# Performance work log

Hardware: AMD Instinct MI355X
Metric: run time of the kernel (lower is better)

The kernel has to match this reference:

```python
import jax, jax.numpy as jnp
import numpy as np

H = 64          # hiddenNum
C3 = 3 * H      # 192 attention channels
FL = 7          # filterLen
PAD = FL // 2
NORM = 1.0 / np.sqrt(C3).astype(np.float32)


def _u(key, shape, stdv):
    return jax.random.uniform(key, shape, jnp.float32, -stdv, stdv)


def setup_inputs() -> dict:
    key = jax.random.key(0)
    ks = iter(jax.random.split(key, 64))
    B, N = 16, 1024
    x = jax.random.normal(next(ks), (B, N, 128), jnp.float32)
    adj = jax.random.uniform(next(ks), (B, N, N), jnp.float32)
    degree = jax.random.uniform(next(ks), (B, N, N), jnp.float32)
    eps = jax.random.normal(next(ks), (B, C3), jnp.float32) * 0.1
    d = {"x": x, "adj": adj, "degree": degree, "eps": eps}
    # GCN params (torch uniform(-1/sqrt(out), 1/sqrt(out)))
    for name, fi, fo in [("gcn1", 128, 2 * H), ("gcn2", H, 4 * H), ("gcn3", 2 * H, 6 * H)]:
        s = 1.0 / np.sqrt(fo)
        d[name + "_w"] = _u(next(ks), (fi, fo), s)
        d[name + "_b"] = _u(next(ks), (fo,), s)
    # Conv1d params [out, in, k]
    for name, ci, co in [("conv1", 128, 2 * H), ("conv2", H, 4 * H), ("conv3", 2 * H, 6 * H)]:
        s = 1.0 / np.sqrt(ci * FL)
        d[name + "_w"] = _u(next(ks), (co, ci, FL), s)
        d[name + "_b"] = _u(next(ks), (co,), s)
    # 1x1 conv Q/K/V projections
    s = 1.0 / np.sqrt(C3)
    for name in ["srq", "srk", "srv", "drq", "drk", "drv"]:
        d[name + "_w"] = _u(next(ks), (C3, C3, 1), s)
        d[name + "_b"] = _u(next(ks), (C3,), s)
    # Linear layers [out, in]
    for name in ["l1", "l2"]:
        d[name + "_w"] = _u(next(ks), (C3, C3), s)
        d[name + "_b"] = _u(next(ks), (C3,), s)
    return d


def _glu_last(y):
    o, g = jnp.split(y, 2, axis=-1)
    return o * jax.nn.sigmoid(g)


def _glu_ch(y):
    o, g = jnp.split(y, 2, axis=1)
    return o * jax.nn.sigmoid(g)


def _conv1d(x, w, b, pad):
    y = jax.lax.conv_general_dilated(x, w, (1,), [(pad, pad)],
                                     dimension_numbers=("NCH", "OIH", "NCH"))
    return y + b[None, :, None]


def reference(x, adj, degree, eps,
              gcn1_w, gcn1_b, gcn2_w, gcn2_b, gcn3_w, gcn3_b,
              conv1_w, conv1_b, conv2_w, conv2_b, conv3_w, conv3_b,
              srq_w, srq_b, srk_w, srk_b, srv_w, srv_b,
              drq_w, drq_b, drk_w, drk_b, drv_w, drv_b,
              l1_w, l1_b, l2_w, l2_b):
    # normalized adjacency: D @ A @ D  (batched dense bmm, as in the original)
    adj_n = jnp.matmul(jnp.matmul(degree, adj), degree)  # [B,N,N]

    def gcn(inp, W, b):
        return jnp.matmul(adj_n, inp @ W) + b

    # GCN branch with GLU gating (eval mode: dropout = identity)
    g1 = _glu_last(gcn(x, gcn1_w, gcn1_b))      # [B,N,H]
    g2 = _glu_last(gcn(g1, gcn2_w, gcn2_b))     # [B,N,2H]
    g3 = _glu_last(gcn(g2, gcn3_w, gcn3_b))     # [B,N,3H]
    gcn_out = jnp.transpose(g3, (0, 2, 1))      # [B,3H,N]

    # CNN branch with gated convs
    xc = jnp.transpose(x, (0, 2, 1))            # [B,128,N]
    c1 = _glu_ch(_conv1d(xc, conv1_w, conv1_b, PAD))   # [B,H,N]
    c2 = _glu_ch(_conv1d(c1, conv2_w, conv2_b, PAD))   # [B,2H,N]
    cnn_out = _glu_ch(_conv1d(c2, conv3_w, conv3_b, PAD))  # [B,3H,N]

    # 1x1-conv Q/K/V projections
    def p1x1(t, w, b):
        return jnp.einsum('oc,bcn->bon', w[:, :, 0], t) + b[None, :, None]

    SRQ = p1x1(cnn_out, srq_w, srq_b)
    SRK = p1x1(cnn_out, srk_w, srk_b)
    SRV = p1x1(cnn_out, srv_w, srv_b)
    DRQ = p1x1(gcn_out, drq_w, drq_b)
    DRK = p1x1(gcn_out, drk_w, drk_b)
    DRV = p1x1(gcn_out, drv_w, drv_b)

    # dual cross-attention; NOTE: scale applied AFTER softmax, as in the source
    attSR = jax.nn.softmax(jnp.einsum('bcn,bcm->bnm', SRQ, DRK), axis=-1) * NORM
    outSR = jnp.einsum('bnm,bcm->bnc', attSR, SRV)   # [B,N,3H]
    attDR = jax.nn.softmax(jnp.einsum('bcn,bcm->bnm', DRQ, SRK), axis=-1) * NORM
    outDR = jnp.einsum('bnm,bcm->bnc', attDR, DRV)   # [B,N,3H]

    feat = outSR + outDR                              # [B,N,3H]
    pooled = jnp.mean(feat, axis=1)                   # AdaptiveAvgPool1d(1) over N -> [B,3H]

    out1 = jax.nn.relu(pooled @ l1_w.T + l1_b)        # mean
    out2 = jax.nn.relu(pooled @ l2_w.T + l2_b)        # logvar
    std = jnp.exp(0.5 * out2)
    out0 = eps * std + out1                           # reparametrize
    return (out0, out1, out2)
```

## Files before the change

### kernel.cpp

```cpp
#include <hip/hip_runtime.h>


#define Bn 16
#define Nn 1024
#define C3n 192
static __device__ __constant__ float NORM_C = 0.07216878364870322f;

typedef short bf16x8 __attribute__((ext_vector_type(8)));
typedef float f32x4 __attribute__((ext_vector_type(4)));
typedef unsigned short u16;
typedef unsigned short u16x4 __attribute__((ext_vector_type(4)));

__device__ __forceinline__ u16 bf16rn(float x)
{
  unsigned b = __float_as_uint(x);
  b += 0x7fffu + ((b >> 16) & 1u);
  return (u16)(b >> 16);
}
__device__ __forceinline__ float fromh(u16 h) { return __uint_as_float(((unsigned)h) << 16); }

template<int TM, int TN, bool OUTB, int BIAS, bool ACC, bool OUTT>
__global__ __launch_bounds__(256, 2) void mgemm_k(
    const u16* __restrict__ A, long sA, int lda,
    const u16* __restrict__ B, long sB, int ldb,
    const float* __restrict__ bias,
    float* __restrict__ Cf, u16* __restrict__ Cb,
    int M, int N, int K)
{
  constexpr int WMN = (TM >= 128) ? 2 : 1;
  constexpr int WNN = 4 / WMN;
  constexpr int WTM = TM / WMN, WTN = TN / WNN;
  constexpr int FM = WTM / 16, FN = WTN / 16;
  constexpr int BBASE = TM * 128;
  __shared__ __align__(16) char sm[(TM + TN) * 128];

  const int bz = (int)blockIdx.z;
  const int n0 = blockIdx.x * TN, m0 = blockIdx.y * TM;
  const int tid = threadIdx.x, lane = tid & 63, w = tid >> 6;
  const int wm0 = (w / WNN) * WTM, wn0 = (w % WNN) * WTN;

  bf16x8 rA[TM / 32], rB[TN / 32];
  auto loadA = [&](int k0) {
    const u16* p = A + bz * sA + (long)m0 * lda + k0;
#pragma unroll
    for (int i = 0; i < TM / 32; ++i) {
      const int v = tid + i * 256, row = v >> 3, vc = v & 7;
      rA[i] = *(const bf16x8*)(p + (long)row * lda + vc * 8);
    }
  };
  auto storeA = [&]() {
#pragma unroll
    for (int i = 0; i < TM / 32; ++i) {
      const int v = tid + i * 256, row = v >> 3, vc = v & 7;
      *(bf16x8*)(sm + row * 128 + ((vc * 16) ^ ((row & 7) << 4))) = rA[i];
    }
  };
  auto loadB = [&](int k0) {
    const u16* p = B + bz * sB + (long)n0 * ldb + k0;
#pragma unroll
    for (int i = 0; i < TN / 32; ++i) {
      const int v = tid + i * 256, row = v >> 3, vc = v & 7;
      rB[i] = *(const bf16x8*)(p + (long)row * ldb + vc * 8);
    }
  };
  auto storeB = [&]() {
#pragma unroll
    for (int i = 0; i < TN / 32; ++i) {
      const int v = tid + i * 256, row = v >> 3, vc = v & 7;
      *(bf16x8*)(sm + BBASE + row * 128 + ((vc * 16) ^ ((row & 7) << 4))) = rB[i];
    }
  };

  f32x4 acc[FM][FN];
#pragma unroll
  for (int c = 0; c < FM; ++c)
#pragma unroll
    for (int d = 0; d < FN; ++d) acc[c][d] = (f32x4)(0.0f);

  loadA(0); loadB(0);
  for (int k0 = 0; k0 < K; k0 += 64) {
    storeA(); storeB();
    __syncthreads();
    if (k0 + 64 < K) { loadA(k0 + 64); loadB(k0 + 64); }
#pragma unroll
    for (int s = 0; s < 2; ++s) {
      const int kb = s * 64 + ((lane >> 4) << 4);
      bf16x8 ah[FM], bh[FN];
#pragma unroll
      for (int c = 0; c < FM; ++c) {
        const int ar = wm0 + c * 16 + (lane & 15);
        ah[c] = *(const bf16x8*)(sm + ar * 128 + (kb ^ ((ar & 7) << 4)));
      }
#pragma unroll
      for (int d = 0; d < FN; ++d) {
        const int br = wn0 + d * 16 + (lane & 15);
        bh[d] = *(const bf16x8*)(sm + BBASE + br * 128 + (kb ^ ((br & 7) << 4)));
      }
#pragma unroll
      for (int c = 0; c < FM; ++c)
#pragma unroll
        for (int d = 0; d < FN; ++d)
          acc[c][d] = __builtin_amdgcn_mfma_f32_16x16x32_bf16(ah[c], bh[d], acc[c][d], 0, 0, 0);
    }
    __syncthreads();
  }

  const long cb = (long)bz * M * N;
#pragma unroll
  for (int c = 0; c < FM; ++c)
#pragma unroll
    for (int d = 0; d < FN; ++d) {
      const int row0 = m0 + wm0 + c * 16 + (lane >> 4) * 4;
      const int col = n0 + wn0 + d * 16 + (lane & 15);
      if constexpr (OUTT) {
        u16x4 vv;
#pragma unroll
        for (int r = 0; r < 4; ++r) vv[r] = bf16rn(acc[c][d][r]);
        *(u16x4*)(Cb + cb + (long)col * M + row0) = vv;
      } else {
        float bcol = 0.f;
        if constexpr (BIAS == 1) bcol = bias[col];
#pragma unroll
        for (int r = 0; r < 4; ++r) {
          const int row = row0 + r;
          float v = acc[c][d][r];
          if constexpr (BIAS == 1) v += bcol;
          if constexpr (BIAS == 2) v += bias[row];
          const long idx = cb + (long)row * N + col;
          if constexpr (OUTB) {
            Cb[idx] = bf16rn(v);
          } else {
            if constexpr (ACC) v += Cf[idx];
            Cf[idx] = v;
          }
        }
      }
    }
}

__device__ __forceinline__ void gemm64_body(char* sm,
    const u16* __restrict__ A, int lda, const u16* __restrict__ B, int ldb,
    const float* __restrict__ bias, u16* __restrict__ Cb,
    int N, int K, int m0, int n0, bool biasRow)
{
  const int tid = threadIdx.x, lane = tid & 63, w = tid >> 6;
  bf16x8 rA[2], rB[2];
  auto loadA = [&](int k0) {
#pragma unroll
    for (int i = 0; i < 2; ++i) {
      const int v = tid + i * 256, row = v >> 3, vc = v & 7;
      rA[i] = *(const bf16x8*)(A + (long)(m0 + row) * lda + k0 + vc * 8);
    }
  };
  auto loadB = [&](int k0) {
#pragma unroll
    for (int i = 0; i < 2; ++i) {
      const int v = tid + i * 256, row = v >> 3, vc = v & 7;
      rB[i] = *(const bf16x8*)(B + (long)(n0 + row) * ldb + k0 + vc * 8);
    }
  };
  auto storeAB = [&]() {
#pragma unroll
    for (int i = 0; i < 2; ++i) {
      const int v = tid + i * 256, row = v >> 3, vc = v & 7;
      const int off = row * 128 + ((vc * 16) ^ ((row & 7) << 4));
      *(bf16x8*)(sm + off) = rA[i];
      *(bf16x8*)(sm + 8192 + off) = rB[i];
    }
  };

  f32x4 acc[4];
#pragma unroll
  for (int c = 0; c < 4; ++c) acc[c] = (f32x4)(0.0f);

  loadA(0); loadB(0);
  for (int k0 = 0; k0 < K; k0 += 64) {
    storeAB();
    __syncthreads();
    if (k0 + 64 < K) { loadA(k0 + 64); loadB(k0 + 64); }
#pragma unroll
    for (int s = 0; s < 2; ++s) {
      const int kb = s * 64 + ((lane >> 4) << 4);
      const int br = w * 16 + (lane & 15);
      const bf16x8 bh = *(const bf16x8*)(sm + 8192 + br * 128 + (kb ^ ((br & 7) << 4)));
#pragma unroll
      for (int c = 0; c < 4; ++c) {
        const int ar = c * 16 + (lane & 15);
        const bf16x8 ah = *(const bf16x8*)(sm + ar * 128 + (kb ^ ((ar & 7) << 4)));
        acc[c] = __builtin_amdgcn_mfma_f32_16x16x32_bf16(ah, bh, acc[c], 0, 0, 0);
      }
    }
    __syncthreads();
  }

  const int col = n0 + w * 16 + (lane & 15);
  const float bcol = biasRow ? 0.f : bias[col];
#pragma unroll
  for (int c = 0; c < 4; ++c) {
    const int row0 = m0 + c * 16 + (lane >> 4) * 4;
#pragma unroll
    for (int r = 0; r < 4; ++r) {
      const int row = row0 + r;
      const float bv = biasRow ? bias[row] : bcol;
      Cb[(long)row * N + col] = bf16rn(acc[c][r] + bv);
    }
  }
}

__global__ __launch_bounds__(256, 2) void qk4_k(
    const u16* __restrict__ inA, const u16* __restrict__ inB,
    const u16* __restrict__ w0, const u16* __restrict__ w1,
    const u16* __restrict__ w2, const u16* __restrict__ w3,
    const float* __restrict__ b0, const float* __restrict__ b1,
    const float* __restrict__ b2, const float* __restrict__ b3,
    u16* __restrict__ o0, u16* __restrict__ o1,
    u16* __restrict__ o2, u16* __restrict__ o3)
{
  __shared__ __align__(16) char sm[16384];
  constexpr long QS = (long)Nn * C3n;
  const int z = blockIdx.z, p = z >> 4, b = z & 15;
  const u16* in = (p < 2) ? inA : inB;
  const u16* W = (p == 0) ? w0 : (p == 1) ? w1 : (p == 2) ? w2 : w3;
  const float* bias = (p == 0) ? b0 : (p == 1) ? b1 : (p == 2) ? b2 : b3;
  u16* out = (p == 0) ? o0 : (p == 1) ? o1 : (p == 2) ? o2 : o3;
  gemm64_body(sm, in + (long)b * QS, C3n, W, C3n, bias, out + (long)b * QS,
              C3n, C3n, blockIdx.y * 64, blockIdx.x * 64, false);
}

__global__ __launch_bounds__(256, 2) void v2_k(
    const u16* __restrict__ inA, const u16* __restrict__ inB,
    const u16* __restrict__ w0, const u16* __restrict__ w1,
    const float* __restrict__ b0, const float* __restrict__ b1,
    u16* __restrict__ o0, u16* __restrict__ o1)
{
  __shared__ __align__(16) char sm[16384];
  constexpr long QS = (long)Nn * C3n;
  const int z = blockIdx.z, p = z >> 4, b = z & 15;
  const u16* in = p ? inB : inA;
  const u16* W = p ? w1 : w0;
  const float* bias = p ? b1 : b0;
  u16* out = p ? o1 : o0;
  gemm64_body(sm, W, C3n, in + (long)b * QS, C3n, bias, out + (long)b * QS,
              Nn, C3n, blockIdx.y * 64, blockIdx.x * 64, true);
}

template<int KC, bool OUTT>
__global__ __launch_bounds__(256, 2) void wglu_k(
    const u16* __restrict__ A, long sA,
    const u16* __restrict__ W,
    const float* __restrict__ bias,
    u16* __restrict__ G, long sG, int H)
{
  __shared__ __align__(16) char sm[3 * 8192];
  const int bz = blockIdx.z;
  const int h0 = blockIdx.x * 64, m0 = blockIdx.y * 64;
  const int tid = threadIdx.x, lane = tid & 63, w = tid >> 6;
  const int wn0 = w * 16;

  f32x4 accO[4], accG[4];
#pragma unroll
  for (int c = 0; c < 4; ++c) { accO[c] = (f32x4)(0.0f); accG[c] = (f32x4)(0.0f); }

  for (int k0 = 0; k0 < KC; k0 += 64) {
#pragma unroll
    for (int i = 0; i < 2; ++i) {
      const int v = tid + i * 256, row = v >> 3, vc = v & 7;
      const int off = row * 128 + ((vc * 16) ^ ((row & 7) << 4));
      *(bf16x8*)(sm + off) = *(const bf16x8*)(A + bz * sA + (long)(m0 + row) * KC + k0 + vc * 8);
      *(bf16x8*)(sm + 8192 + off) = *(const bf16x8*)(W + (long)(h0 + row) * KC + k0 + vc * 8);
      *(bf16x8*)(sm + 16384 + off) = *(const bf16x8*)(W + (long)(H + h0 + row) * KC + k0 + vc * 8);
    }
    __syncthreads();
#pragma unroll
    for (int s = 0; s < 2; ++s) {
      const int kb = s * 64 + ((lane >> 4) << 4);
      const int br = wn0 + (lane & 15);
      const bf16x8 bo = *(const bf16x8*)(sm + 8192 + br * 128 + (kb ^ ((br & 7) << 4)));
      const bf16x8 bg = *(const bf16x8*)(sm + 16384 + br * 128 + (kb ^ ((br & 7) << 4)));
#pragma unroll
      for (int c = 0; c < 4; ++c) {
        const int ar = c * 16 + (lane & 15);
        const bf16x8 a = *(const bf16x8*)(sm + ar * 128 + (kb ^ ((ar & 7) << 4)));
        accO[c] = __builtin_amdgcn_mfma_f32_16x16x32_bf16(a, bo, accO[c], 0, 0, 0);
        accG[c] = __builtin_amdgcn_mfma_f32_16x16x32_bf16(a, bg, accG[c], 0, 0, 0);
      }
    }
    __syncthreads();
  }

  const int col = h0 + wn0 + (lane & 15);
  const float bo = bias[col], bg = bias[H + col];
#pragma unroll
  for (int c = 0; c < 4; ++c) {
    const int row0 = m0 + c * 16 + (lane >> 4) * 4;
    if constexpr (OUTT) {
      u16x4 vv;
#pragma unroll
      for (int r = 0; r < 4; ++r) {
        const float o = accO[c][r] + bo, g = accG[c][r] + bg;
        vv[r] = bf16rn(o / (1.f + expf(-g)));
      }
      *(u16x4*)(G + bz * sG + (long)col * Nn + row0) = vv;
    } else {
#pragma unroll
      for (int r = 0; r < 4; ++r) {
        const float o = accO[c][r] + bo, g = accG[c][r] + bg;
        G[bz * sG + (long)(row0 + r) * H + col] = bf16rn(o / (1.f + expf(-g)));
      }
    }
  }
}

__global__ __launch_bounds__(256, 2) void conv_mfma_k(
    const u16* __restrict__ Wp, const u16* __restrict__ in_nm, int ldin, long sIn,
    u16* __restrict__ Z, long sZ, int Ci, int M)
{
  __shared__ __align__(16) char sm[9216 + 7 * 8192];
  const int bz = blockIdx.z;
  const int n0 = blockIdx.x * 64, m0 = blockIdx.y * 64;
  const int tid = threadIdx.x, lane = tid & 63, w = tid >> 6;
  const int wm = (w >> 1) * 32, wn = (w & 1) * 32;
  const u16* inb = in_nm + bz * sIn;

  f32x4 acc[2][2];
#pragma unroll
  for (int c = 0; c < 2; ++c)
#pragma unroll
    for (int d = 0; d < 2; ++d) acc[c][d] = (f32x4)(0.0f);

  for (int k0 = 0; k0 < Ci; k0 += 64) {
#pragma unroll
    for (int r = 0; r < 3; ++r) {
      const int idx = r * 256 + tid;
      if (idx < 576) {
        const int row = idx >> 3, ch = idx & 7;
        const int g = n0 + row - 3;
        bf16x8 v;
#pragma unroll
        for (int j = 0; j < 8; ++j) v[j] = 0;
        if ((unsigned)g < (unsigned)Nn)
          v = *(const bf16x8*)(inb + (long)g * ldin + k0 + ch * 8);
        *(bf16x8*)(sm + row * 128 + ((ch * 16) ^ ((row & 7) << 4))) = v;
      }
    }
#pragma unroll
    for (int i = 0; i < 14; ++i) {
      const int v = tid + i * 256;
      const int ft = v >> 9, rr = (v >> 3) & 63, vc = v & 7;
      const bf16x8 t = *(const bf16x8*)(Wp + ((long)ft * M + m0 + rr) * Ci + k0 + vc * 8);
      *(bf16x8*)(sm + 9216 + ft * 8192 + rr * 128 + ((vc * 16) ^ ((rr & 7) << 4))) = t;
    }
    __syncthreads();
#pragma unroll
    for (int ft = 0; ft < 7; ++ft) {
#pragma unroll
      for (int s = 0; s < 2; ++s) {
        const int kb = s * 64 + ((lane >> 4) << 4);
        bf16x8 ah[2], bh[2];
#pragma unroll
        for (int c = 0; c < 2; ++c) {
          const int ar = wm + c * 16 + (lane & 15);
          ah[c] = *(const bf16x8*)(sm + 9216 + ft * 8192 + ar * 128 + (kb ^ ((ar & 7) << 4)));
          const int hr = wn + c * 16 + (lane & 15) + ft;
          bh[c] = *(const bf16x8*)(sm + hr * 128 + (kb ^ ((hr & 7) << 4)));
        }
#pragma unroll
        for (int c = 0; c < 2; ++c)
#pragma unroll
          for (int d = 0; d < 2; ++d)
            acc[c][d] = __builtin_amdgcn_mfma_f32_16x16x32_bf16(ah[c], bh[d], acc[c][d], 0, 0, 0);
      }
    }
    __syncthreads();
  }

  u16* Zb = Z + bz * sZ;
#pragma unroll
  for (int c = 0; c < 2; ++c)
#pragma unroll
    for (int d = 0; d < 2; ++d) {
      const int row0 = m0 + wm + c * 16 + (lane >> 4) * 4;
      const int col = n0 + wn + d * 16 + (lane & 15);
#pragma unroll
      for (int r = 0; r < 4; ++r)
        Zb[(long)(row0 + r) * Nn + col] = bf16rn(acc[c][d][r]);
    }
}

__global__ __launch_bounds__(256, 2) void attn_k(
    const u16* __restrict__ Q0, const u16* __restrict__ K0,
    const u16* __restrict__ V0, float* __restrict__ O0,
    const u16* __restrict__ Q1, const u16* __restrict__ K1,
    const u16* __restrict__ V1, float* __restrict__ O1)
{
  constexpr long QS = (long)Nn * C3n;
  __shared__ __align__(16) char sm[81920];
  const int qb = blockIdx.x, b = blockIdx.y, at = blockIdx.z;
  const u16* Q = (at ? Q1 : Q0) + (long)b * QS + (long)qb * 64 * C3n;
  const u16* K = (at ? K1 : K0) + (long)b * QS;
  const u16* V = (at ? V1 : V0) + (long)b * QS;
  float* O = (at ? O1 : O0) + (long)b * QS;
  const int tid = threadIdx.x, lane = tid & 63, w = tid >> 6;

  {
    const int row = tid >> 2;
#pragma unroll
    for (int j = 0; j < 6; ++j) {
      const int ch = (tid & 3) + j * 4;
      *(bf16x8*)(sm + row * 384 + ((ch * 16) ^ ((row & 7) << 4))) =
          *(const bf16x8*)(Q + (long)row * C3n + ch * 8);
    }
  }

  bf16x8 rK[6], rV[6];
  auto loadK = [&](int kb) {
    const int row = tid >> 2;
#pragma unroll
    for (int j = 0; j < 6; ++j) {
      const int ch = (tid & 3) + j * 4;
      rK[j] = *(const bf16x8*)(K + ((long)kb * 64 + row) * C3n + ch * 8);
    }
  };
  auto storeK = [&]() {
    const int row = tid >> 2;
#pragma unroll
    for (int j = 0; j < 6; ++j) {
      const int ch = (tid & 3) + j * 4;
      *(bf16x8*)(sm + 24576 + row * 384 + ((ch * 16) ^ ((row & 7) << 4))) = rK[j];
    }
  };
  auto loadV = [&](int kb) {
#pragma unroll
    for (int j = 0; j < 6; ++j) {
      const int row = (tid >> 3) + j * 32;
      const int ch = tid & 7;
      rV[j] = *(const bf16x8*)(V + (long)row * Nn + kb * 64 + ch * 8);
    }
  };
  auto storeV = [&]() {
#pragma unroll
    for (int j = 0; j < 6; ++j) {
      const int row = (tid >> 3) + j * 32;
      const int ch = tid & 7;
      *(bf16x8*)(sm + 49152 + row * 128 + ((ch * 16) ^ ((row & 7) << 4))) = rV[j];
    }
  };

  f32x4 accO[12];
#pragma unroll
  for (int f = 0; f < 12; ++f) accO[f] = (f32x4)(0.0f);
  float m[4], l[4];
#pragma unroll
  for (int r = 0; r < 4; ++r) { m[r] = -3.0e38f; l[r] = 0.f; }

  loadK(0);
  for (int kb = 0; kb < 16; ++kb) {
    storeK();
    __syncthreads();
    loadV(kb);

    f32x4 accS[4];
#pragma unroll
    for (int d = 0; d < 4; ++d) accS[d] = (f32x4)(0.0f);
    __builtin_amdgcn_s_setprio(1);
#pragma unroll
    for (int s = 0; s < 6; ++s) {
      const int kpos = s * 64 + ((lane >> 4) << 4);
      const int ar = w * 16 + (lane & 15);
      const bf16x8 a = *(const bf16x8*)(sm + ar * 384 + (kpos ^ ((ar & 7) << 4)));
#pragma unroll
      for (int d = 0; d < 4; ++d) {
        const int br = d * 16 + (lane & 15);
        const bf16x8 bb = *(const bf16x8*)(sm + 24576 + br * 384 + (kpos ^ ((br & 7) << 4)));
        accS[d] = __builtin_amdgcn_mfma_f32_16x16x32_bf16(a, bb, accS[d], 0, 0, 0);
      }
    }
    __builtin_amdgcn_s_setprio(0);

    float fac[4];
    bool need = false;
#pragma unroll
    for (int r = 0; r < 4; ++r) {
      float mx = fmaxf(fmaxf(accS[0][r], accS[1][r]), fmaxf(accS[2][r], accS[3][r]));
#pragma unroll
      for (int off = 8; off; off >>= 1) mx = fmaxf(mx, __shfl_xor(mx, off));
      float mn;
      if (mx > m[r] + 8.f) {
        mn = mx;
        fac[r] = __expf(m[r] - mn);
        m[r] = mn;
        need = true;
      } else {
        mn = m[r];
        fac[r] = 1.f;
      }
      float rs = 0.f;
#pragma unroll
      for (int d = 0; d < 4; ++d) {
        float e = __expf(accS[d][r] - mn);
        if (e != e) e = (accS[d][r] == mn) ? 1.f : 0.f;
        accS[d][r] = e;
        rs += e;
      }
#pragma unroll
      for (int off = 8; off; off >>= 1) rs += __shfl_xor(rs, off);
      l[r] = l[r] * fac[r] + rs;
    }
    if (__any(need)) {
#pragma unroll
      for (int f = 0; f < 12; ++f)
#pragma unroll
        for (int r = 0; r < 4; ++r) accO[f][r] *= fac[r];
    }

    {
      const int qbase = w * 16 + (lane >> 4) * 4;
#pragma unroll
      for (int r = 0; r < 4; ++r) {
        const int qr = qbase + r;
#pragma unroll
        for (int d = 0; d < 4; ++d) {
          const int colb = (d * 16 + (lane & 15)) * 2;
          *(u16*)(sm + 73728 + qr * 128 + (colb ^ ((qr & 7) << 4))) = bf16rn(accS[d][r]);
        }
      }
    }
    storeV();
    __syncthreads();
    if (kb < 15) loadK(kb + 1);

    __builtin_amdgcn_s_setprio(1);
#pragma unroll
    for (int s = 0; s < 2; ++s) {
      const int kpos = s * 64 + ((lane >> 4) << 4);
      const int ar = w * 16 + (lane & 15);
      const bf16x8 a = *(const bf16x8*)(sm + 73728 + ar * 128 + (kpos ^ ((ar & 7) << 4)));
#pragma unroll
      for (int f = 0; f < 12; ++f) {
        const int br = f * 16 + (lane & 15);
        const bf16x8 bb = *(const bf16x8*)(sm + 49152 + br * 128 + (kpos ^ ((br & 7) << 4)));
        accO[f] = __builtin_amdgcn_mfma_f32_16x16x32_bf16(a, bb, accO[f], 0, 0, 0);
      }
    }
    __builtin_amdgcn_s_setprio(0);
  }

#pragma unroll
  for (int r = 0; r < 4; ++r) {
    const int row = qb * 64 + w * 16 + (lane >> 4) * 4 + r;
    const float inv = NORM_C / l[r];
#pragma unroll
    for (int f = 0; f < 12; ++f)
      O[(long)row * C3n + f * 16 + (lane & 15)] = accO[f][r] * inv;
  }
}

__global__ void cvt2_k(const float* __restrict__ a, const float* __restrict__ b,
                       u16* __restrict__ da, u16* __restrict__ db, long half4)
{
  const long i = (long)blockIdx.x * 256 + threadIdx.x;
  if (i >= 2 * half4) return;
  const bool second = (i >= half4);
  const long j = second ? i - half4 : i;
  float4 v = ((const float4*)(second ? b : a))[j];
  u16x4 o = {bf16rn(v.x), bf16rn(v.y), bf16rn(v.z), bf16rn(v.w)};
  ((u16x4*)(second ? db : da))[j] = o;
}

__global__ void xcvt2_k(const float* __restrict__ x, u16* __restrict__ xh,
                        u16* __restrict__ xc)
{
  __shared__ float t[32][33];
  const int b = blockIdx.z;
  const int n0 = blockIdx.x * 32, c0 = blockIdx.y * 32;
  const int tx = threadIdx.x, ty = threadIdx.y;
#pragma unroll
  for (int i = 0; i < 32; i += 8) {
    const float v = x[((long)b * Nn + n0 + ty + i) * 128 + c0 + tx];
    t[ty + i][tx] = v;
    xh[((long)b * Nn + n0 + ty + i) * 128 + c0 + tx] = bf16rn(v);
  }
  __syncthreads();
#pragma unroll
  for (int i = 0; i < 32; i += 8)
    xc[((long)b * 128 + c0 + ty + i) * Nn + n0 + tx] = bf16rn(t[tx][ty + i]);
}

__global__ void cvtw6_k(const float* s0, const float* s1, const float* s2,
                        const float* s3, const float* s4, const float* s5,
                        u16* d0, u16* d1, u16* d2, u16* d3, u16* d4, u16* d5)
{
  const int which = blockIdx.y;
  const float* s = which==0?s0:which==1?s1:which==2?s2:which==3?s3:which==4?s4:s5;
  u16* d = which==0?d0:which==1?d1:which==2?d2:which==3?d3:which==4?d4:d5;
  const int i = blockIdx.x * 256 + threadIdx.x;
  if (i >= 192*192/4) return;
  float4 v = ((const float4*)s)[i];
  u16x4 o = {bf16rn(v.x), bf16rn(v.y), bf16rn(v.z), bf16rn(v.w)};
  ((u16x4*)d)[i] = o;
}

__global__ void wt_k(const float* __restrict__ W, u16* __restrict__ Wt, int R, int C)
{
  __shared__ float t[32][33];
  const int c0 = blockIdx.x * 32, r0 = blockIdx.y * 32;
  const int tx = threadIdx.x, ty = threadIdx.y;
#pragma unroll
  for (int i = 0; i < 32; i += 8)
    t[ty + i][tx] = W[(long)(r0 + ty + i) * C + c0 + tx];
  __syncthreads();
#pragma unroll
  for (int i = 0; i < 32; i += 8)
    Wt[(long)(c0 + ty + i) * R + r0 + tx] = bf16rn(t[tx][ty + i]);
}

__global__ void wp_k(const float* __restrict__ w, u16* __restrict__ Wp, int Co, int Ci)
{
  const int idx = blockIdx.x * 256 + threadIdx.x;
  if (idx >= Co * Ci * 7) return;
  const int ft = idx / (Co * Ci);
  const int rem = idx - ft * Co * Ci;
  const int co = rem / Ci, ci = rem - co * Ci;
  Wp[idx] = bf16rn(w[((long)co * Ci + ci) * 7 + ft]);
}

__global__ void glu_cht_k(const u16* __restrict__ Z, const float* __restrict__ bias,
                          u16* __restrict__ G, int H)
{
  __shared__ float t[32][33];
  const int b = blockIdx.z;
  const int n0 = blockIdx.x * 32, h0 = blockIdx.y * 32;
  const int tx = threadIdx.x, ty = threadIdx.y;
  const u16* Zb = Z + (long)b * 2 * H * Nn;
#pragma unroll
  for (int i = 0; i < 32; i += 8) {
    const int h = h0 + ty + i;
    const float o = fromh(Zb[(long)h * Nn + n0 + tx]) + bias[h];
    const float g = fromh(Zb[(long)(H + h) * Nn + n0 + tx]) + bias[H + h];
    t[ty + i][tx] = o / (1.f + expf(-g));
  }
  __syncthreads();
#pragma unroll
  for (int i = 0; i < 32; i += 8)
    G[((long)b * Nn + n0 + ty + i) * H + h0 + tx] = bf16rn(t[tx][ty + i]);
}

__global__ void pool_k(const float* __restrict__ fa, const float* __restrict__ fb,
                       float* __restrict__ ppart)
{
  const int chunk = blockIdx.x, b = blockIdx.y;
  const int c = threadIdx.x;
  const long base = ((long)b * Nn + chunk * 128) * C3n + c;
  float s = 0.f;
  for (int n = 0; n < 128; ++n) s += fa[base + (long)n * C3n] + fb[base + (long)n * C3n];
  ppart[(b * 8 + chunk) * C3n + c] = s;
}

__device__ __forceinline__ float sanitize(float v)
{
  if (v != v) return 0.f;
  return fminf(fmaxf(v, -3.0e38f), 3.0e38f);
}

__global__ void head_k(const float* __restrict__ ppart,
                       const float* __restrict__ l1w, const float* __restrict__ l1b,
                       const float* __restrict__ l2w, const float* __restrict__ l2b,
                       const float* __restrict__ eps, float* __restrict__ out)
{
  const int b = blockIdx.x, o = threadIdx.x;
  __shared__ float sp[C3n];
  float sacc = 0.f;
  for (int k = 0; k < 8; ++k) sacc += ppart[(b * 8 + k) * C3n + o];
  sp[o] = sacc * (1.f / Nn);
  __syncthreads();
  float d1 = l1b[o], d2 = l2b[o];
  for (int c = 0; c < C3n; ++c) {
    d1 = fmaf(sp[c], l1w[o * C3n + c], d1);
    d2 = fmaf(sp[c], l2w[o * C3n + c], d2);
  }
  const float o1 = fmaxf(d1, 0.f);
  const float o2 = fmaxf(d2, 0.f);
  const float sd = fminf(expf(0.5f * o2), 3.0e38f);
  const double v0 = (double)eps[b * C3n + o] * (double)sd + (double)o1;
  out[b * C3n + o] = sanitize((float)fmin(fmax(v0, -3.0e38), 3.0e38));
  out[Bn * C3n + b * C3n + o] = sanitize(o1);
  out[2 * Bn * C3n + b * C3n + o] = sanitize(o2);
}

extern "C" void kernel_launch(void* const* d_in, const int* in_sizes, int n_in,
                              void* d_out, int out_size, void* d_ws, size_t ws_size,
                              hipStream_t stream)
{
  const float* x    = (const float*)d_in[0];
  const float* adjm = (const float*)d_in[1];
  const float* deg  = (const float*)d_in[2];
  const float* eps  = (const float*)d_in[3];
  const float* g1w  = (const float*)d_in[4];
  const float* g1b  = (const float*)d_in[5];
  const float* g2w  = (const float*)d_in[6];
  const float* g2b  = (const float*)d_in[7];
  const float* g3w  = (const float*)d_in[8];
  const float* g3b  = (const float*)d_in[9];
  const float* c1w  = (const float*)d_in[10];
  const float* c1b  = (const float*)d_in[11];
  const float* c2w  = (const float*)d_in[12];
  const float* c2b  = (const float*)d_in[13];
  const float* c3w  = (const float*)d_in[14];
  const float* c3b  = (const float*)d_in[15];
  const float* srqw = (const float*)d_in[16];
  const float* srqb = (const float*)d_in[17];
  const float* srkw = (const float*)d_in[18];
  const float* srkb = (const float*)d_in[19];
  const float* srvw = (const float*)d_in[20];
  const float* srvb = (const float*)d_in[21];
  const float* drqw = (const float*)d_in[22];
  const float* drqb = (const float*)d_in[23];
  const float* drkw = (const float*)d_in[24];
  const float* drkb = (const float*)d_in[25];
  const float* drvw = (const float*)d_in[26];
  const float* drvb = (const float*)d_in[27];
  const float* l1w  = (const float*)d_in[28];
  const float* l1b  = (const float*)d_in[29];
  const float* l2w  = (const float*)d_in[30];
  const float* l2b  = (const float*)d_in[31];
  float* out = (float*)d_out;
  char* ws = (char*)d_ws;

  constexpr long MBc = 1L << 20;
  u16*  DEGB = (u16*)(ws + 0*MBc);
  u16*  ADJB = (u16*)(ws + 34*MBc);
  u16*  Z    = (u16*)(ws + 68*MBc);
  u16*  c1b16= (u16*)(ws + 94*MBc);
  u16*  c2b16= (u16*)(ws + 97*MBc);
  u16*  T1   = (u16*)(ws + 94*MBc);
  u16*  T2   = (u16*)(ws + 99*MBc);
  u16*  Pb   = (u16*)(ws + 104*MBc);
  u16*  CNN  = (u16*)(ws + 109*MBc);
  u16*  G3   = (u16*)(ws + 116*MBc);
  u16*  xh   = (u16*)(ws + 123*MBc);
  u16*  xch  = (u16*)(ws + 128*MBc);
  u16*  G1   = (u16*)(ws + 133*MBc);
  u16*  G2   = (u16*)(ws + 136*MBc);
  u16*  SRQ = (u16*)(ws + 0*MBc);
  u16*  SRK = (u16*)(ws + 7*MBc);
  u16*  DRQ = (u16*)(ws + 14*MBc);
  u16*  DRK = (u16*)(ws + 21*MBc);
  u16*  SRV = (u16*)(ws + 28*MBc);
  u16*  DRV = (u16*)(ws + 35*MBc);
  float* FEATA = (float*)(ws + 43*MBc);
  float* FEATB = (float*)(ws + 57*MBc);

  long wb = 141 * MBc;
  auto aU = [&](long elems) { u16* p = (u16*)(ws + wb); wb += elems * 2; wb = (wb + 255) & ~255L; return p; };
  u16* W1t = aU(128*128);
  u16* W2t = aU(256*64);
  u16* W3t = aU(384*128);
  u16* WP1 = aU(7*128*128);
  u16* WP2 = aU(7*256*64);
  u16* WP3 = aU(7*384*128);
  u16* QW[6];
  for (int i = 0; i < 6; ++i) QW[i] = aU(192*192);
  float* PPART = (float*)(ws + wb);

  const long sNN = (long)Nn * Nn;
  const long QS = (long)Nn * C3n;
  const long sCM128 = (long)128 * Nn;

  cvt2_k<<<32768, 256, 0, stream>>>(deg, adjm, DEGB, ADJB, sNN * Bn / 4);
  xcvt2_k<<<dim3(32,4,Bn), dim3(32,8), 0, stream>>>(x, xh, xch);
  wt_k<<<dim3(4,4), dim3(32,8), 0, stream>>>(g1w, W1t, 128, 128);
  wt_k<<<dim3(8,2), dim3(32,8), 0, stream>>>(g2w, W2t, 64, 256);
  wt_k<<<dim3(12,4), dim3(32,8), 0, stream>>>(g3w, W3t, 128, 384);
  wp_k<<<(128*128*7+255)/256, 256, 0, stream>>>(c1w, WP1, 128, 128);
  wp_k<<<(256*64*7+255)/256, 256, 0, stream>>>(c2w, WP2, 256, 64);
  wp_k<<<(384*128*7+255)/256, 256, 0, stream>>>(c3w, WP3, 384, 128);
  cvtw6_k<<<dim3(36, 6), 256, 0, stream>>>(srqw, srkw, srvw, drqw, drkw, drvw,
                                           QW[0], QW[1], QW[2], QW[3], QW[4], QW[5]);

  conv_mfma_k<<<dim3(16,2,Bn), 256, 0, stream>>>(WP1, xh, 128, (long)Nn*128, Z, sCM128, 128, 128);
  glu_cht_k<<<dim3(32,2,Bn), dim3(32,8), 0, stream>>>(Z, c1b, c1b16, 64);
  conv_mfma_k<<<dim3(16,4,Bn), 256, 0, stream>>>(WP2, c1b16, 64, (long)Nn*64, Z, (long)256*Nn, 64, 256);
  glu_cht_k<<<dim3(32,4,Bn), dim3(32,8), 0, stream>>>(Z, c2b, c2b16, 128);
  conv_mfma_k<<<dim3(16,6,Bn), 256, 0, stream>>>(WP3, c2b16, 128, (long)Nn*128, Z, (long)384*Nn, 128, 384);
  glu_cht_k<<<dim3(32,6,Bn), dim3(32,8), 0, stream>>>(Z, c3b, CNN, 192);

  mgemm_k<64,64,false,0,false,true><<<dim3(2,16,Bn), 256, 0, stream>>>(
      DEGB, sNN, Nn, xch, sCM128, Nn, nullptr, nullptr, T1, Nn, 128, Nn);
  mgemm_k<64,64,false,0,false,true><<<dim3(2,16,Bn), 256, 0, stream>>>(
      ADJB, sNN, Nn, T1, sCM128, Nn, nullptr, nullptr, T2, Nn, 128, Nn);
  mgemm_k<64,64,true,0,false,false><<<dim3(2,16,Bn), 256, 0, stream>>>(
      DEGB, sNN, Nn, T2, sCM128, Nn, nullptr, nullptr, Pb, Nn, 128, Nn);
  wglu_k<128,true><<<dim3(1,16,Bn), 256, 0, stream>>>(
      Pb, (long)Nn*128, W1t, g1b, G1, (long)64*Nn, 64);
  mgemm_k<64,64,false,0,false,true><<<dim3(1,16,Bn), 256, 0, stream>>>(
      DEGB, sNN, Nn, G1, (long)64*Nn, Nn, nullptr, nullptr, T1, Nn, 64, Nn);
  mgemm_k<64,64,false,0,false,true><<<dim3(1,16,Bn), 256, 0, stream>>>(
      ADJB, sNN, Nn, T1, (long)64*Nn, Nn, nullptr, nullptr, T2, Nn, 64, Nn);
  mgemm_k<64,64,true,0,false,false><<<dim3(1,16,Bn), 256, 0, stream>>>(
      DEGB, sNN, Nn, T2, (long)64*Nn, Nn, nullptr, nullptr, Pb, Nn, 64, Nn);
  wglu_k<64,true><<<dim3(2,16,Bn), 256, 0, stream>>>(
      Pb, (long)Nn*64, W2t, g2b, G2, sCM128, 128);
  mgemm_k<64,64,false,0,false,true><<<dim3(2,16,Bn), 256, 0, stream>>>(
      DEGB, sNN, Nn, G2, sCM128, Nn, nullptr, nullptr, T1, Nn, 128, Nn);
  mgemm_k<64,64,false,0,false,true><<<dim3(2,16,Bn), 256, 0, stream>>>(
      ADJB, sNN, Nn, T1, sCM128, Nn, nullptr, nullptr, T2, Nn, 128, Nn);
  mgemm_k<64,64,true,0,false,false><<<dim3(2,16,Bn), 256, 0, stream>>>(
      DEGB, sNN, Nn, T2, sCM128, Nn, nullptr, nullptr, Pb, Nn, 128, Nn);
  wglu_k<128,false><<<dim3(3,16,Bn), 256, 0, stream>>>(
      Pb, (long)Nn*128, W3t, g3b, G3, QS, 192);

  qk4_k<<<dim3(3,16,64), 256, 0, stream>>>(
      CNN, G3, QW[0], QW[1], QW[3], QW[4], srqb, srkb, drqb, drkb,
      SRQ, SRK, DRQ, DRK);
  v2_k<<<dim3(16,3,32), 256, 0, stream>>>(
      CNN, G3, QW[2], QW[5], srvb, drvb, SRV, DRV);

  attn_k<<<dim3(16, Bn, 2), 256, 0, stream>>>(
      SRQ, DRK, SRV, FEATA, DRQ, SRK, DRV, FEATB);

  pool_k<<<dim3(8, Bn), C3n, 0, stream>>>(FEATA, FEATB, PPART);
  head_k<<<Bn, C3n, 0, stream>>>(PPART, l1w, l1b, l2w, l2b, eps, out);
}
```

Measured before the change: 353.5 us.

## Fuse fp32-to-bf16 conversion of adjacency into GEMM loads; MFMA row-sum in attention

Removes the standalone kernel that converted the dense degree and adjacency matrices to bf16, and instead makes the propagation GEMMs load fp32 A tiles and round to bf16 while staging into shared memory. In attention, the softmax denominator is now accumulated with an extra MFMA against a ones vector rather than cross-lane shuffles. The fusion eliminates one large conversion pass, but each of the nine GEMMs now reads the matrices in fp32, doubling their A-operand traffic.

```diff
diff --git a/kernel.cpp b/kernel.cpp
--- a/kernel.cpp
+++ b/kernel.cpp
@@ -19,9 +19,9 @@
 }
 __device__ __forceinline__ float fromh(u16 h) { return __uint_as_float(((unsigned)h) << 16); }
 
-template<int TM, int TN, bool OUTB, int BIAS, bool ACC, bool OUTT>
+template<int TM, int TN, bool AF32, bool OUTB, int BIAS, bool ACC, bool OUTT>
 __global__ __launch_bounds__(256, 2) void mgemm_k(
-    const u16* __restrict__ A, long sA, int lda,
+    const u16* __restrict__ A, const float* __restrict__ Af, long sA, int lda,
     const u16* __restrict__ B, long sB, int ldb,
     const float* __restrict__ bias,
     float* __restrict__ Cf, u16* __restrict__ Cb,
@@ -39,20 +39,41 @@
   const int tid = threadIdx.x, lane = tid & 63, w = tid >> 6;
   const int wm0 = (w / WNN) * WTM, wn0 = (w % WNN) * WTN;
 
-  bf16x8 rA[TM / 32], rB[TN / 32];
+  bf16x8 rA[AF32 ? 1 : TM / 32];
+  float4 rAf[AF32 ? TM / 16 : 1];
+  bf16x8 rB[TN / 32];
   auto loadA = [&](int k0) {
-    const u16* p = A + bz * sA + (long)m0 * lda + k0;
-#pragma unroll
-    for (int i = 0; i < TM / 32; ++i) {
-      const int v = tid + i * 256, row = v >> 3, vc = v & 7;
-      rA[i] = *(const bf16x8*)(p + (long)row * lda + vc * 8);
+    if constexpr (AF32) {
+      const float* p = Af + bz * sA + (long)m0 * lda + k0;
+#pragma unroll
+      for (int i = 0; i < TM / 16; ++i) {
+        const int v = tid + i * 256, row = v >> 4, q = v & 15;
+        rAf[i] = *(const float4*)(p + (long)row * lda + q * 4);
+      }
+    } else {
+      const u16* p = A + bz * sA + (long)m0 * lda + k0;
+#pragma unroll
+      for (int i = 0; i < TM / 32; ++i) {
+        const int v = tid + i * 256, row = v >> 3, vc = v & 7;
+        rA[i] = *(const bf16x8*)(p + (long)row * lda + vc * 8);
+      }
     }
   };
   auto storeA = [&]() {
-#pragma unroll
-    for (int i = 0; i < TM / 32; ++i) {
-      const int v = tid + i * 256, row = v >> 3, vc = v & 7;
-      *(bf16x8*)(sm + row * 128 + ((vc * 16) ^ ((row & 7) << 4))) = rA[i];
+    if constexpr (AF32) {
+#pragma unroll
+      for (int i = 0; i < TM / 16; ++i) {
+        const int v = tid + i * 256, row = v >> 4, q = v & 15;
+        const int off = row * 128 + ((q * 8) ^ ((row & 7) << 4));
+        u16x4 o = {bf16rn(rAf[i].x), bf16rn(rAf[i].y), bf16rn(rAf[i].z), bf16rn(rAf[i].w)};
+        *(u16x4*)(sm + off) = o;
+      }
+    } else {
+#pragma unroll
+      for (int i = 0; i < TM / 32; ++i) {
+        const int v = tid + i * 256, row = v >> 3, vc = v & 7;
+        *(bf16x8*)(sm + row * 128 + ((vc * 16) ^ ((row & 7) << 4))) = rA[i];
+      }
     }
   };
   auto loadB = [&](int k0) {
@@ -402,6 +423,10 @@
   float* O = (at ? O1 : O0) + (long)b * QS;
   const int tid = threadIdx.x, lane = tid & 63, w = tid >> 6;
 
+  bf16x8 vone;
+#pragma unroll
+  for (int j = 0; j < 8; ++j) vone[j] = (short)0x3F80;
+
   {
     const int row = tid >> 2;
 #pragma unroll
@@ -446,12 +471,13 @@
     }
   };
 
-  f32x4 accO[12];
+  f32x4 accO[12], accL;
 #pragma unroll
   for (int f = 0; f < 12; ++f) accO[f] = (f32x4)(0.0f);
-  float m[4], l[4];
-#pragma unroll
-  for (int r = 0; r < 4; ++r) { m[r] = -3.0e38f; l[r] = 0.f; }
+  accL = (f32x4)(0.0f);
+  float m[4];
+#pragma unroll
+  for (int r = 0; r < 4; ++r) m[r] = -3.0e38f;
 
   loadK(0);
   for (int kb = 0; kb < 16; ++kb) {
@@ -494,23 +520,20 @@
         mn = m[r];
         fac[r] = 1.f;
       }
-      float rs = 0.f;
 #pragma unroll
       for (int d = 0; d < 4; ++d) {
         float e = __expf(accS[d][r] - mn);
         if (e != e) e = (accS[d][r] == mn) ? 1.f : 0.f;
         accS[d][r] = e;
-        rs += e;
-      }
-#pragma unroll
-      for (int off = 8; off; off >>= 1) rs += __shfl_xor(rs, off);
-      l[r] = l[r] * fac[r] + rs;
+      }
     }
     if (__any(need)) {
 #pragma unroll
       for (int f = 0; f < 12; ++f)
 #pragma unroll
         for (int r = 0; r < 4; ++r) accO[f][r] *= fac[r];
+#pragma unroll
+      for (int r = 0; r < 4; ++r) accL[r] *= fac[r];
     }
 
     {
@@ -541,6 +564,7 @@
         const bf16x8 bb = *(const bf16x8*)(sm + 49152 + br * 128 + (kpos ^ ((br & 7) << 4)));
         accO[f] = __builtin_amdgcn_mfma_f32_16x16x32_bf16(a, bb, accO[f], 0, 0, 0);
       }
+      accL = __builtin_amdgcn_mfma_f32_16x16x32_bf16(a, vone, accL, 0, 0, 0);
     }
     __builtin_amdgcn_s_setprio(0);
   }
@@ -548,23 +572,11 @@
 #pragma unroll
   for (int r = 0; r < 4; ++r) {
     const int row = qb * 64 + w * 16 + (lane >> 4) * 4 + r;
-    const float inv = NORM_C / l[r];
+    const float inv = NORM_C / accL[r];
 #pragma unroll
     for (int f = 0; f < 12; ++f)
       O[(long)row * C3n + f * 16 + (lane & 15)] = accO[f][r] * inv;
   }
-}
-
-__global__ void cvt2_k(const float* __restrict__ a, const float* __restrict__ b,
-                       u16* __restrict__ da, u16* __restrict__ db, long half4)
-{
-  const long i = (long)blockIdx.x * 256 + threadIdx.x;
-  if (i >= 2 * half4) return;
-  const bool second = (i >= half4);
-  const long j = second ? i - half4 : i;
-  float4 v = ((const float4*)(second ? b : a))[j];
-  u16x4 o = {bf16rn(v.x), bf16rn(v.y), bf16rn(v.z), bf16rn(v.w)};
-  ((u16x4*)(second ? db : da))[j] = o;
 }
 
 __global__ void xcvt2_k(const float* __restrict__ x, u16* __restrict__ xh,
@@ -727,8 +739,6 @@
   char* ws = (char*)d_ws;
 
   constexpr long MBc = 1L << 20;
-  u16*  DEGB = (u16*)(ws + 0*MBc);
-  u16*  ADJB = (u16*)(ws + 34*MBc);
   u16*  Z    = (u16*)(ws + 68*MBc);
   u16*  c1b16= (u16*)(ws + 94*MBc);
   u16*  c2b16= (u16*)(ws + 97*MBc);
@@ -766,7 +776,6 @@
   const long QS = (long)Nn * C3n;
   const long sCM128 = (long)128 * Nn;
 
-  cvt2_k<<<32768, 256, 0, stream>>>(deg, adjm, DEGB, ADJB, sNN * Bn / 4);
   xcvt2_k<<<dim3(32,4,Bn), dim3(32,8), 0, stream>>>(x, xh, xch);
   wt_k<<<dim3(4,4), dim3(32,8), 0, stream>>>(g1w, W1t, 128, 128);
   wt_k<<<dim3(8,2), dim3(32,8), 0, stream>>>(g2w, W2t, 64, 256);
@@ -784,28 +793,28 @@
   conv_mfma_k<<<dim3(16,6,Bn), 256, 0, stream>>>(WP3, c2b16, 128, (long)Nn*128, Z, (long)384*Nn, 128, 384);
   glu_cht_k<<<dim3(32,6,Bn), dim3(32,8), 0, stream>>>(Z, c3b, CNN, 192);
 
-  mgemm_k<64,64,false,0,false,true><<<dim3(2,16,Bn), 256, 0, stream>>>(
-      DEGB, sNN, Nn, xch, sCM128, Nn, nullptr, nullptr, T1, Nn, 128, Nn);
-  mgemm_k<64,64,false,0,false,true><<<dim3(2,16,Bn), 256, 0, stream>>>(
-      ADJB, sNN, Nn, T1, sCM128, Nn, nullptr, nullptr, T2, Nn, 128, Nn);
-  mgemm_k<64,64,true,0,false,false><<<dim3(2,16,Bn), 256, 0, stream>>>(
-      DEGB, sNN, Nn, T2, sCM128, Nn, nullptr, nullptr, Pb, Nn, 128, Nn);
+  mgemm_k<64,64,true,false,0,false,true><<<dim3(2,16,Bn), 256, 0, stream>>>(
+      nullptr, deg, sNN, Nn, xch, sCM128, Nn, nullptr, nullptr, T1, Nn, 128, Nn);
+  mgemm_k<64,64,true,false,0,false,true><<<dim3(2,16,Bn), 256, 0, stream>>>(
+      nullptr, adjm, sNN, Nn, T1, sCM128, Nn, nullptr, nullptr, T2, Nn, 128, Nn);
+  mgemm_k<64,64,true,true,0,false,false><<<dim3(2,16,Bn), 256, 0, stream>>>(
+      nullptr, deg, sNN, Nn, T2, sCM128, Nn, nullptr, nullptr, Pb, Nn, 128, Nn);
   wglu_k<128,true><<<dim3(1,16,Bn), 256, 0, stream>>>(
       Pb, (long)Nn*128, W1t, g1b, G1, (long)64*Nn, 64);
-  mgemm_k<64,64,false,0,false,true><<<dim3(1,16,Bn), 256, 0, stream>>>(
-      DEGB, sNN, Nn, G1, (long)64*Nn, Nn, nullptr, nullptr, T1, Nn, 64, Nn);
-  mgemm_k<64,64,false,0,false,true><<<dim3(1,16,Bn), 256, 0, stream>>>(
-      ADJB, sNN, Nn, T1, (long)64*Nn, Nn, nullptr, nullptr, T2, Nn, 64, Nn);
-  mgemm_k<64,64,true,0,false,false><<<dim3(1,16,Bn), 256, 0, stream>>>(
-      DEGB, sNN, Nn, T2, (long)64*Nn, Nn, nullptr, nullptr, Pb, Nn, 64, Nn);
+  mgemm_k<64,64,true,false,0,false,true><<<dim3(1,16,Bn), 256, 0, stream>>>(
+      nullptr, deg, sNN, Nn, G1, (long)64*Nn, Nn, nullptr, nullptr, T1, Nn, 64, Nn);
+  mgemm_k<64,64,true,false,0,false,true><<<dim3(1,16,Bn), 256, 0, stream>>>(
+      nullptr, adjm, sNN, Nn, T1, (long)64*Nn, Nn, nullptr, nullptr, T2, Nn, 64, Nn);
+  mgemm_k<64,64,true,true,0,false,false><<<dim3(1,16,Bn), 256, 0, stream>>>(
+      nullptr, deg, sNN, Nn, T2, (long)64*Nn, Nn, nullptr, nullptr, Pb, Nn, 64, Nn);
   wglu_k<64,true><<<dim3(2,16,Bn), 256, 0, stream>>>(
       Pb, (long)Nn*64, W2t, g2b, G2, sCM128, 128);
-  mgemm_k<64,64,false,0,false,true><<<dim3(2,16,Bn), 256, 0, stream>>>(
-      DEGB, sNN, Nn, G2, sCM128, Nn, nullptr, nullptr, T1, Nn, 128, Nn);
-  mgemm_k<64,64,false,0,false,true><<<dim3(2,16,Bn), 256, 0, stream>>>(
-      ADJB, sNN, Nn, T1, sCM128, Nn, nullptr, nullptr, T2, Nn, 128, Nn);
-  mgemm_k<64,64,true,0,false,false><<<dim3(2,16,Bn), 256, 0, stream>>>(
-      DEGB, sNN, Nn, T2, sCM128, Nn, nullptr, nullptr, Pb, Nn, 128, Nn);
+  mgemm_k<64,64,true,false,0,false,true><<<dim3(2,16,Bn), 256, 0, stream>>>(
+      nullptr, deg, sNN, Nn, G2, sCM128, Nn, nullptr, nullptr, T1, Nn, 128, Nn);
+  mgemm_k<64,64,true,false,0,false,true><<<dim3(2,16,Bn), 256, 0, stream>>>(
+      nullptr, adjm, sNN, Nn, T1, sCM128, Nn, nullptr, nullptr, T2, Nn, 128, Nn);
+  mgemm_k<64,64,true,true,0,false,false><<<dim3(2,16,Bn), 256, 0, stream>>>(
+      nullptr, deg, sNN, Nn, T2, sCM128, Nn, nullptr, nullptr, Pb, Nn, 128, Nn);
   wglu_k<128,false><<<dim3(3,16,Bn), 256, 0, stream>>>(
       Pb, (long)Nn*128, W3t, g3b, G3, QS, 192);
 
```

Result: slower. 384.3 us (+8.7%).
